# Performance work log

Measured on AMD Instinct MI355X. Metric: run time of the kernel, lower is better.

Reference implementation:

```python
import jax, jax.numpy as jnp
import numpy as np

N = 4096  # input_features == output_features == transform length (power of 2)


def _fft(x, twiddle_factors):
    """Faithful vectorized form of the module's radix-2 butterfly network.

    x: (N, D) complex64. twiddle_factors: (N, D) float32 (the learned weights).
    Original loop: for each stage `step`, for each block, for r in [0, half):
        k = r * (N // step)
        temp = exp(-2j*pi*k/N * twiddle_factors[k]) * x[j + half]
        new x[j + half] = x[j] - temp ; new x[j] = x[j] + temp
    Blocks are independent, so each stage is a single batched butterfly.
    """
    n = x.shape[0]
    # initial permutation: index xor with N//2 (as written in the source; not full bit-reversal)
    x = x[jnp.bitwise_xor(jnp.arange(n), n // 2)]
    step = 2
    while step <= n:  # log2(N) stages, fixed small Python loop
        half = step // 2
        k = jnp.arange(half) * (n // step)                      # (half,)
        phase = (-2.0 * jnp.pi) * (k[:, None].astype(jnp.float32) / n) * twiddle_factors[k]
        tw = jnp.exp(1j * phase)                                # (half, D) complex64
        xr = x.reshape(n // step, step, -1)                     # (blocks, step, D)
        top = xr[:, :half]
        bot = xr[:, half:]
        temp = tw[None] * bot                                   # (blocks, half, D)
        x = jnp.concatenate([top + temp, top - temp], axis=1).reshape(n, -1)
        step *= 2
    return x


def setup_inputs() -> dict:
    key = jax.random.key(0)
    kx, kw = jax.random.split(key)
    x = jax.random.normal(kx, (N, N), dtype=jnp.float32)
    weights = jax.random.normal(kw, (N, N), dtype=jnp.float32)  # nn.Parameter(randn(out, in))
    return {"x": x, "weights": weights}


def reference(x, weights):
    # input_features == output_features -> no pad / no truncation branch taken
    return _fft(x.astype(jnp.complex64), weights)
```

## Files before the change

### kernel.cpp

```cpp
#include <hip/hip_runtime.h>

#define INV_N (1.0f / 4096.0f)

__device__ __forceinline__ void bf(float& ar, float& ai, float& br, float& bi,
                                   float s, float cs) {
    float tr = cs * br - s * bi;
    float ti = cs * bi + s * br;
    br = ar - tr; bi = ai - ti;
    ar = ar + tr; ai = ai + ti;
}

__device__ __forceinline__ void tw(int k, float wk, float* s, float* cs) {
    float rev = (float)k * (-INV_N) * wk;
    rev = __builtin_amdgcn_fractf(rev);
    *s  = __builtin_amdgcn_sinf(rev);
    *cs = __builtin_amdgcn_cosf(rev);
}

__device__ __forceinline__ void exchange(float2* tile, float (&ar)[16],
                                         float (&ai)[16], int pb, int c) {
#pragma unroll
    for (int par = 0; par < 2; ++par) {
#pragma unroll
        for (int m = 0; m < 16; ++m) {
            if (((pb + (m >> 2) + (m & 3)) & 1) == par) {
                int srow = (pb << 3) + (((m >> 2) << 1) | ((m & 3) >> 1));
                tile[srow * 64 + c] = make_float2(ar[m], ai[m]);
            }
        }
        __syncthreads();
#pragma unroll
        for (int m = 0; m < 16; ++m) {
            if (((pb + (m >> 2) + (m & 3)) & 1) == par) {
                int srow = ((m >> 2) << 3) + ((m & 3) << 1) + (pb >> 1);
                float2 v = tile[srow * 64 + c];
                ar[m] = v.x; ai[m] = v.y;
            }
        }
        if (par == 0) __syncthreads();
    }
}

__global__ __launch_bounds__(256) void fft_lo(const float* __restrict__ x,
                                              const float* __restrict__ w,
                                              float2* __restrict__ dst2,
                                              unsigned dst_lim2) {
    __shared__ __align__(16) float2 tile[32 * 64];
    const int t   = threadIdx.x;
    const int c   = t & 63;
    const int pb  = t >> 6;
    const int c0  = (blockIdx.x & 63) << 6;
    const int r0  = (blockIdx.x >> 6) << 6;
    const int src_r0 = r0 ^ 2048;
    const int col = c0 + c;

    float wp1[7];
#pragma unroll
    for (int i = 0; i < 7; ++i)
        wp1[i] = w[(size_t)(256 * (i + 1)) * 4096 + col];
    float w2a[4], w2b[8];
#pragma unroll
    for (int i = 0; i < 4; ++i)
        w2a[i] = w[(size_t)((pb + 4 * i) * 128) * 4096 + col];
#pragma unroll
    for (int i = 0; i < 8; ++i)
        w2b[i] = w[(size_t)((pb + 4 * i) * 64) * 4096 + col];

    float ar[16], ai[16];
#pragma unroll
    for (int m = 0; m < 16; ++m) {
        ar[m] = __builtin_nontemporal_load(&x[(size_t)(src_r0 + 16 * pb + m) * 4096 + col]);
        ai[m] = 0.f;
    }

    float s1[8], c1[8];
    s1[0] = 0.f; c1[0] = 1.f;
#pragma unroll
    for (int i = 1; i < 8; ++i)
        tw(256 * i, wp1[i - 1], &s1[i], &c1[i]);

#pragma unroll
    for (int h = 1; h <= 8; h <<= 1) {
        const int step = h << 1;
#pragma unroll
        for (int r = 0; r < h; ++r) {
            const int ti = r * (8 / h);
            const float s = s1[ti], cs = c1[ti];
#pragma unroll
            for (int b = 0; b < 8 / h; ++b) {
                const int mt = b * step + r;
                bf(ar[mt], ai[mt], ar[mt + h], ai[mt + h], s, cs);
            }
        }
    }

    float s2a[4], c2a[4], s2b[8], c2b[8];
#pragma unroll
    for (int i = 0; i < 4; ++i)
        tw((pb + 4 * i) * 128, w2a[i], &s2a[i], &c2a[i]);
#pragma unroll
    for (int i = 0; i < 8; ++i)
        tw((pb + 4 * i) * 64, w2b[i], &s2b[i], &c2b[i]);

    exchange(tile, ar, ai, pb, c);

#pragma unroll
    for (int rm = 0; rm < 4; ++rm) {
#pragma unroll
        for (int b = 0; b < 2; ++b) {
            const int mt = b * 8 + rm;
            bf(ar[mt], ai[mt], ar[mt + 4], ai[mt + 4], s2a[rm], c2a[rm]);
        }
    }
#pragma unroll
    for (int m = 0; m < 8; ++m)
        bf(ar[m], ai[m], ar[m + 8], ai[m + 8], s2b[m], c2b[m]);

#pragma unroll
    for (int m = 0; m < 16; ++m) {
        size_t gi = (size_t)(r0 + pb + 4 * m) * 4096 + col;
        if (gi < dst_lim2) dst2[gi] = make_float2(ar[m], ai[m]);
    }
}

template <int REAL_OUT>
__global__ __launch_bounds__(256) void fft_hi(const float* __restrict__ w,
                                              const float2* __restrict__ src2,
                                              float2* __restrict__ dstc,
                                              float* __restrict__ dstr,
                                              unsigned dst_lim) {
    __shared__ __align__(16) float2 tile[32 * 64];
    const int t    = threadIdx.x;
    const int c    = t & 63;
    const int pb   = t >> 6;
    const int c0   = (blockIdx.x & 63) << 6;
    const int rres = blockIdx.x >> 6;
    const int col  = c0 + c;

    float wp1, wp2[2], wp4[4], wp8[8];
    wp1 = w[(size_t)(rres * 32) * 4096 + col];
#pragma unroll
    for (int r = 0; r < 2; ++r)
        wp2[r] = w[(size_t)((rres + 64 * r) * 16) * 4096 + col];
#pragma unroll
    for (int r = 0; r < 4; ++r)
        wp4[r] = w[(size_t)((rres + 64 * r) * 8) * 4096 + col];
#pragma unroll
    for (int r = 0; r < 8; ++r)
        wp8[r] = w[(size_t)((rres + 64 * r) * 4) * 4096 + col];
    float w2a[4], w2b[8];
#pragma unroll
    for (int i = 0; i < 4; ++i)
        w2a[i] = w[(size_t)((rres + 64 * (pb + 4 * i)) * 2) * 4096 + col];
#pragma unroll
    for (int i = 0; i < 8; ++i)
        w2b[i] = w[(size_t)(rres + 64 * (pb + 4 * i)) * 4096 + col];

    float ar[16], ai[16];
#pragma unroll
    for (int m = 0; m < 16; ++m) {
        float2 v = src2[(size_t)(rres + 64 * (16 * pb + m)) * 4096 + col];
        ar[m] = v.x; ai[m] = v.y;
    }

    {
        float s, cs;
        tw(rres * 32, wp1, &s, &cs);
#pragma unroll
        for (int b = 0; b < 8; ++b)
            bf(ar[2 * b], ai[2 * b], ar[2 * b + 1], ai[2 * b + 1], s, cs);
    }
#pragma unroll
    for (int r = 0; r < 2; ++r) {
        float s, cs;
        tw((rres + 64 * r) * 16, wp2[r], &s, &cs);
#pragma unroll
        for (int b = 0; b < 4; ++b) {
            const int mt = b * 4 + r;
            bf(ar[mt], ai[mt], ar[mt + 2], ai[mt + 2], s, cs);
        }
    }
#pragma unroll
    for (int r = 0; r < 4; ++r) {
        float s, cs;
        tw((rres + 64 * r) * 8, wp4[r], &s, &cs);
#pragma unroll
        for (int b = 0; b < 2; ++b) {
            const int mt = b * 8 + r;
            bf(ar[mt], ai[mt], ar[mt + 4], ai[mt + 4], s, cs);
        }
    }
#pragma unroll
    for (int r = 0; r < 8; ++r) {
        float s, cs;
        tw((rres + 64 * r) * 4, wp8[r], &s, &cs);
        bf(ar[r], ai[r], ar[r + 8], ai[r + 8], s, cs);
    }

    float s2a[4], c2a[4], s2b[8], c2b[8];
#pragma unroll
    for (int i = 0; i < 4; ++i)
        tw((rres + 64 * (pb + 4 * i)) * 2, w2a[i], &s2a[i], &c2a[i]);
#pragma unroll
    for (int i = 0; i < 8; ++i)
        tw(rres + 64 * (pb + 4 * i), w2b[i], &s2b[i], &c2b[i]);

    exchange(tile, ar, ai, pb, c);

#pragma unroll
    for (int rm = 0; rm < 4; ++rm) {
#pragma unroll
        for (int b = 0; b < 2; ++b) {
            const int mt = b * 8 + rm;
            bf(ar[mt], ai[mt], ar[mt + 4], ai[mt + 4], s2a[rm], c2a[rm]);
        }
    }
#pragma unroll
    for (int m = 0; m < 8; ++m)
        bf(ar[m], ai[m], ar[m + 8], ai[m + 8], s2b[m], c2b[m]);

    if (REAL_OUT) {
#pragma unroll
        for (int m = 0; m < 16; ++m) {
            size_t gi = (size_t)(rres + 64 * (pb + 4 * m)) * 4096 + col;
            if (gi < dst_lim) __builtin_nontemporal_store(ar[m], &dstr[gi]);
        }
    } else {
#pragma unroll
        for (int m = 0; m < 16; ++m) {
            size_t gi = (size_t)(rres + 64 * (pb + 4 * m)) * 4096 + col;
            if (gi < dst_lim) dstc[gi] = make_float2(ar[m], ai[m]);
        }
    }
}

extern "C" void kernel_launch(void* const* d_in, const int* in_sizes, int n_in,
                              void* d_out, int out_size, void* d_ws, size_t ws_size,
                              hipStream_t stream) {
    const float* x = (const float*)d_in[0];
    const float* w = (const float*)d_in[1];
    const long long NN = 4096LL * 4096LL;

    if ((long long)out_size >= 2 * NN) {
        float2* o2 = (float2*)d_out;
        unsigned lim2 = (unsigned)(out_size / 2);
        fft_lo<<<4096, 256, 0, stream>>>(x, w, o2, lim2);
        fft_hi<0><<<4096, 256, 0, stream>>>(w, o2, o2, nullptr, lim2);
    } else {
        float2* ws2 = (float2*)d_ws;
        unsigned ws_lim2 = (unsigned)(ws_size / 8);
        unsigned out_lim = (unsigned)out_size;
        fft_lo<<<4096, 256, 0, stream>>>(x, w, ws2, ws_lim2);
        fft_hi<1><<<4096, 256, 0, stream>>>(w, (const float2*)ws2, nullptr,
                                            (float*)d_out, out_lim);
    }
}
```

Baseline: 202.1 us.

## Make LDS exchange wave-local to replace block barriers with lgkmcnt waits

Remaps threads so that each wavefront owns 16 columns and all 4 row-groups (pb) of them, and gives each wave a private LDS tile. The transpose exchange then stays inside one wave, so __syncthreads is replaced by s_waitcnt lgkmcnt(0) fences. This removes block-wide barrier stalls between waves. The trade-off is that global accesses now cover 16 contiguous columns per row instead of 64, which gives narrower coalesced segments. Correctness also depends on wave64 lockstep execution and on the inline-asm fence ordering LDS accesses within the wave.

Result: slower. 217.6 us (+7.7%).

```diff
diff --git a/kernel.cpp b/kernel.cpp
--- a/kernel.cpp
+++ b/kernel.cpp
@@ -17,27 +17,29 @@
     *cs = __builtin_amdgcn_cosf(rev);
 }
 
-__device__ __forceinline__ void exchange(float2* tile, float (&ar)[16],
-                                         float (&ai)[16], int pb, int c) {
+#define LDS_FENCE() asm volatile("s_waitcnt lgkmcnt(0)" ::: "memory")
+
+__device__ __forceinline__ void exchange_w(float2* tp, float (&ar)[16],
+                                           float (&ai)[16], int pb, int cl) {
 #pragma unroll
     for (int par = 0; par < 2; ++par) {
 #pragma unroll
         for (int m = 0; m < 16; ++m) {
             if (((pb + (m >> 2) + (m & 3)) & 1) == par) {
                 int srow = (pb << 3) + (((m >> 2) << 1) | ((m & 3) >> 1));
-                tile[srow * 64 + c] = make_float2(ar[m], ai[m]);
+                tp[srow * 16 + cl] = make_float2(ar[m], ai[m]);
             }
         }
-        __syncthreads();
+        LDS_FENCE();
 #pragma unroll
         for (int m = 0; m < 16; ++m) {
             if (((pb + (m >> 2) + (m & 3)) & 1) == par) {
                 int srow = ((m >> 2) << 3) + ((m & 3) << 1) + (pb >> 1);
-                float2 v = tile[srow * 64 + c];
+                float2 v = tp[srow * 16 + cl];
                 ar[m] = v.x; ai[m] = v.y;
             }
         }
-        if (par == 0) __syncthreads();
+        LDS_FENCE();
     }
 }
 
@@ -45,14 +47,16 @@
                                               const float* __restrict__ w,
                                               float2* __restrict__ dst2,
                                               unsigned dst_lim2) {
-    __shared__ __align__(16) float2 tile[32 * 64];
-    const int t   = threadIdx.x;
-    const int c   = t & 63;
-    const int pb  = t >> 6;
-    const int c0  = (blockIdx.x & 63) << 6;
-    const int r0  = (blockIdx.x >> 6) << 6;
+    __shared__ __align__(16) float2 tile[4][32 * 16];
+    const int t    = threadIdx.x;
+    const int wv   = t >> 6;
+    const int lane = t & 63;
+    const int cl   = lane & 15;
+    const int pb   = lane >> 4;
+    const int c0   = (blockIdx.x & 63) << 6;
+    const int r0   = (blockIdx.x >> 6) << 6;
     const int src_r0 = r0 ^ 2048;
-    const int col = c0 + c;
+    const int col  = c0 + wv * 16 + cl;
 
     float wp1[7];
 #pragma unroll
@@ -102,7 +106,7 @@
     for (int i = 0; i < 8; ++i)
         tw((pb + 4 * i) * 64, w2b[i], &s2b[i], &c2b[i]);
 
-    exchange(tile, ar, ai, pb, c);
+    exchange_w(&tile[wv][0], ar, ai, pb, cl);
 
 #pragma unroll
     for (int rm = 0; rm < 4; ++rm) {
@@ -129,13 +133,14 @@
                                               float2* __restrict__ dstc,
                                               float* __restrict__ dstr,
                                               unsigned dst_lim) {
-    __shared__ __align__(16) float2 tile[32 * 64];
+    __shared__ __align__(16) float2 tile[4][32 * 16];
     const int t    = threadIdx.x;
-    const int c    = t & 63;
-    const int pb   = t >> 6;
-    const int c0   = (blockIdx.x & 63) << 6;
+    const int wv   = t >> 6;
+    const int lane = t & 63;
+    const int cl   = lane & 15;
+    const int pb   = lane >> 4;
     const int rres = blockIdx.x >> 6;
-    const int col  = c0 + c;
+    const int col  = ((blockIdx.x & 63) << 6) + wv * 16 + cl;
 
     float wp1, wp2[2], wp4[4], wp8[8];
     wp1 = w[(size_t)(rres * 32) * 4096 + col];
@@ -205,7 +210,7 @@
     for (int i = 0; i < 8; ++i)
         tw(rres + 64 * (pb + 4 * i), w2b[i], &s2b[i], &c2b[i]);
 
-    exchange(tile, ar, ai, pb, c);
+    exchange_w(&tile[wv][0], ar, ai, pb, cl);
 
 #pragma unroll
     for (int rm = 0; rm < 4; ++rm) {
```
